# Kernel optimization log

Hardware: AMD Instinct MI355X
Metric: run time of the kernel (lower is better)

Reference implementation:

```python
import jax, jax.numpy as jnp
import numpy as np

B, T, C = 2, 2048, 2048
N_HEAD = 16
N_KV_HEAD = 16
HEAD_DIM = C // N_HEAD  # 128
KV_LORA = C // 2        # 1024
KV_PE = KV_LORA // 4    # 256
KV_CONTENT = KV_LORA - KV_PE  # 768
EPS = 1.1920929e-07  # torch.finfo(float32).eps, F.rms_norm default


def _rms_norm(x):
    # unlearned RMSNorm over last dim
    return x * jax.lax.rsqrt(jnp.mean(x * x, axis=-1, keepdims=True) + EPS)


def _apply_rotary(x, cos, sin):
    # x: (B,T,H,D); cos,sin: (1,T,1,D/2)
    d = x.shape[-1] // 2
    x1, x2 = x[..., :d], x[..., d:]
    return jnp.concatenate([x1 * cos + x2 * sin, -x1 * sin + x2 * cos], axis=-1)


def setup_inputs() -> dict:
    key = jax.random.key(0)
    ks = jax.random.split(key, 9)
    x = jax.random.normal(ks[0], (B, T, C), dtype=jnp.float32)
    # realistic RoPE tables (values bounded like real cos/sin)
    half = HEAD_DIM // 2
    inv_freq = 1.0 / (10000.0 ** (np.arange(0, half, dtype=np.float32) / half))
    tpos = np.arange(T, dtype=np.float32)
    ang = np.einsum('t,d->td', tpos, inv_freq)
    cos = jnp.asarray(np.cos(ang))[None, :, None, :]
    sin = jnp.asarray(np.sin(ang))[None, :, None, :]
    s = 0.02
    wq_a = jax.random.normal(ks[1], (C, KV_LORA), dtype=jnp.float32) * s
    wq_b = jax.random.normal(ks[2], (KV_LORA, N_HEAD * HEAD_DIM), dtype=jnp.float32) * s
    wkv_a = jax.random.normal(ks[3], (C, KV_LORA), dtype=jnp.float32) * s
    wk_b = jax.random.normal(ks[4], (KV_CONTENT, N_KV_HEAD * HEAD_DIM), dtype=jnp.float32) * s
    wkpe_b = jax.random.normal(ks[5], (KV_PE, N_KV_HEAD * HEAD_DIM), dtype=jnp.float32) * s
    wv_b = jax.random.normal(ks[6], (KV_CONTENT, N_KV_HEAD * HEAD_DIM), dtype=jnp.float32) * s
    wo = jax.random.normal(ks[7], (C, C), dtype=jnp.float32) * s
    return dict(x=x, cos=cos, sin=sin, wq_a=wq_a, wq_b=wq_b, wkv_a=wkv_a,
                wk_b=wk_b, wkpe_b=wkpe_b, wv_b=wv_b, wo=wo)


def reference(x, cos, sin, wq_a, wq_b, wkv_a, wk_b, wkpe_b, wv_b, wo):
    Bx, Tx, Cx = x.shape
    # low-rank Q path
    q = (x @ wq_a) @ wq_b                      # (B,T,H*D)
    q = q.reshape(Bx, Tx, N_HEAD, HEAD_DIM)
    # low-rank KV path with pe/content split
    kv_latent = x @ wkv_a                       # (B,T,KV_LORA)
    kv_pe = kv_latent[..., :KV_PE]
    kv_content = kv_latent[..., KV_PE:]
    k_content = (kv_content @ wk_b).reshape(Bx, Tx, N_KV_HEAD, HEAD_DIM)
    k_pe = (kv_pe @ wkpe_b).reshape(Bx, Tx, N_KV_HEAD, HEAD_DIM)
    k = k_content + _apply_rotary(k_pe, cos, sin)
    v = (kv_content @ wv_b).reshape(Bx, Tx, N_KV_HEAD, HEAD_DIM)
    # QK RMSNorm (unlearned)
    q = _rms_norm(q)
    k = _rms_norm(k)
    # SDPA, causal (kv_cache=None path); n_head == n_kv_head
    qh = q.transpose(0, 2, 1, 3)  # (B,H,T,D)
    kh = k.transpose(0, 2, 1, 3)
    vh = v.transpose(0, 2, 1, 3)
    scale = 1.0 / jnp.sqrt(jnp.asarray(HEAD_DIM, dtype=x.dtype))
    scores = jnp.einsum('bhqd,bhkd->bhqk', qh, kh) * scale
    causal = jnp.tril(jnp.ones((Tx, Tx), dtype=bool))
    scores = jnp.where(causal[None, None], scores, jnp.asarray(-jnp.inf, dtype=scores.dtype))
    probs = jax.nn.softmax(scores, axis=-1)
    y = jnp.einsum('bhqk,bhkd->bhqd', probs, vh)
    y = y.transpose(0, 2, 1, 3).reshape(Bx, Tx, Cx)
    return y @ wo
```

## Files before the change

kernel.cpp:

```cpp
#include <hip/hip_runtime.h>
#include <cstddef>
#include <cstdint>

#define TT 2048
#define HH 16
#define EPSV 1.1920929e-07f
#define QSCALE 0.08838834764831845f
#define LOG2E 1.4426950408889634f
#define THRL 11.0f

typedef short bfv8 __attribute__((ext_vector_type(8)));
typedef float f32x4 __attribute__((ext_vector_type(4)));

__device__ __forceinline__ short f2bf(float f) {
    unsigned u = __builtin_bit_cast(unsigned, f);
    u += 0x7FFFu + ((u >> 16) & 1u);
    return (short)(u >> 16);
}
__device__ __forceinline__ float bf2f(short s) {
    unsigned u = ((unsigned)(unsigned short)s) << 16;
    return __builtin_bit_cast(float, u);
}
__device__ __forceinline__ bfv8 pack8(const float4 a, const float4 b) {
    bfv8 r;
    r[0]=f2bf(a.x); r[1]=f2bf(a.y); r[2]=f2bf(a.z); r[3]=f2bf(a.w);
    r[4]=f2bf(b.x); r[5]=f2bf(b.y); r[6]=f2bf(b.z); r[7]=f2bf(b.w);
    return r;
}
__device__ __forceinline__ void gload16(const void* g, void* l) {
    __builtin_amdgcn_global_load_lds(
        (const __attribute__((address_space(1))) unsigned int*)g,
        (__attribute__((address_space(3))) unsigned int*)l, 16, 0, 0);
}

__global__ __launch_bounds__(256) void convx(const float* __restrict__ src,
                                             short* __restrict__ dst, int n8)
{
    int i = blockIdx.x * blockDim.x + threadIdx.x;
    int stride = gridDim.x * blockDim.x;
    for (; i < n8; i += stride) {
        float4 a = ((const float4*)src)[2*i], b = ((const float4*)src)[2*i+1];
        ((bfv8*)dst)[i] = pack8(a, b);
    }
}

__global__ __launch_bounds__(256) void wtrans(const float* __restrict__ src,
                                              short* __restrict__ dst, int R, int C)
{
    __shared__ short tile[64][72];
    const int tid = threadIdx.x;
    const int r0 = blockIdx.y * 64, c0 = blockIdx.x * 64;
    {
        const int i = tid >> 2, c = (tid & 3) * 16;
        const float* sp = src + ((size_t)(r0 + i)) * C + c0 + c;
        float4 v0 = ((const float4*)sp)[0], v1 = ((const float4*)sp)[1];
        float4 v2 = ((const float4*)sp)[2], v3 = ((const float4*)sp)[3];
        *(bfv8*)&tile[i][c]     = pack8(v0, v1);
        *(bfv8*)&tile[i][c + 8] = pack8(v2, v3);
    }
    __syncthreads();
    {
        const int j = tid >> 2, rc = (tid & 3) * 16;
        bfv8 g0, g1;
#pragma unroll
        for (int jj = 0; jj < 8; ++jj) { g0[jj] = tile[rc + jj][j]; g1[jj] = tile[rc + 8 + jj][j]; }
        short* dp = dst + ((size_t)(c0 + j)) * R + r0 + rc;
        *(bfv8*)dp       = g0;
        *(bfv8*)(dp + 8) = g1;
    }
}

template<int OUT_MODE>
__global__ __launch_bounds__(256) void gemm_bf16(
    const short* __restrict__ A, int lda,
    const short* __restrict__ B, int ldb,
    void* __restrict__ Cptr, int ldc, int K)
{
    __shared__ short As[2][128 * 32];
    __shared__ short Bs[2][128 * 32];
    const int tid = threadIdx.x;
    const int w = tid >> 6, lane = tid & 63;
    const int lr = lane & 15, lg = lane >> 4;
    const int wr = w >> 1, wc = w & 1;
    const size_t bm = (size_t)blockIdx.y * 128, bn = (size_t)blockIdx.x * 128;

    f32x4 acc[4][4] = {};

    const int r0 = tid >> 2, ch = (tid & 3) * 8;
    const short* aB0 = A + (bm + r0) * (size_t)lda + ch;
    const short* aB1 = aB0 + 64 * (size_t)lda;
    const short* bB0 = B + (bn + r0) * (size_t)ldb + ch;
    const short* bB1 = bB0 + 64 * (size_t)ldb;
    const int wof = w * 512;

    gload16(aB0, As[0] + wof);
    gload16(aB1, As[0] + wof + 2048);
    gload16(bB0, Bs[0] + wof);
    gload16(bB1, Bs[0] + wof + 2048);
    __syncthreads();

    int cur = 0;
    for (int k0 = 0; k0 < K; k0 += 32) {
        if (k0 + 32 < K) {
            gload16(aB0 + k0 + 32, As[cur ^ 1] + wof);
            gload16(aB1 + k0 + 32, As[cur ^ 1] + wof + 2048);
            gload16(bB0 + k0 + 32, Bs[cur ^ 1] + wof);
            gload16(bB1 + k0 + 32, Bs[cur ^ 1] + wof + 2048);
        }
        bfv8 af[4], bfr[4];
#pragma unroll
        for (int i = 0; i < 4; ++i) {
            af[i]  = *(const bfv8*)&As[cur][(wr * 64 + i * 16 + lr) * 32 + lg * 8];
            bfr[i] = *(const bfv8*)&Bs[cur][(wc * 64 + i * 16 + lr) * 32 + lg * 8];
        }
#pragma unroll
        for (int i = 0; i < 4; ++i)
#pragma unroll
            for (int j = 0; j < 4; ++j)
                acc[i][j] = __builtin_amdgcn_mfma_f32_16x16x32_bf16(af[i], bfr[j], acc[i][j], 0, 0, 0);
        __syncthreads();
        cur ^= 1;
    }

    const size_t crow = bm + wr * 64 + 4 * lg;
    const size_t ccol = bn + wc * 64 + lr;
#pragma unroll
    for (int i = 0; i < 4; ++i)
#pragma unroll
        for (int j = 0; j < 4; ++j)
#pragma unroll
            for (int r = 0; r < 4; ++r) {
                size_t off = (crow + i * 16 + r) * (size_t)ldc + ccol + j * 16;
                if (OUT_MODE == 0) ((float*)Cptr)[off] = acc[i][j][r];
                else               ((short*)Cptr)[off] = f2bf(acc[i][j][r]);
            }
}

__global__ __launch_bounds__(256) void finalize_k(
    const short* __restrict__ kc, const short* __restrict__ pe,
    const float* __restrict__ cosb, const float* __restrict__ sinb,
    short* __restrict__ kb)
{
    const int gw = blockIdx.x * 4 + (threadIdx.x >> 6);
    const int l = threadIdx.x & 63;
    const int r = gw >> 4, h = gw & 15;
    const int t = r & (TT - 1), b = r >> 11;
    const size_t kcb = (size_t)r * 4096 + h * 128;
    const size_t peb = (size_t)r * 2048 + h * 128;

    float x1 = bf2f(pe[peb + l]), x2 = bf2f(pe[peb + 64 + l]);
    float c = cosb[t * 64 + l], s = sinb[t * 64 + l];
    float lo = bf2f(kc[kcb + l])      + x1 * c + x2 * s;
    float hi = bf2f(kc[kcb + 64 + l]) - x1 * s + x2 * c;

    float ss = lo * lo + hi * hi;
#pragma unroll
    for (int o = 32; o; o >>= 1) ss += __shfl_xor(ss, o);
    float rr = rsqrtf(ss * (1.0f / 128.0f) + EPSV);
    const size_t ob = (((size_t)b * HH + h) * TT + t) * 128;
    kb[ob + l]      = f2bf(lo * rr);
    kb[ob + 64 + l] = f2bf(hi * rr);
}

__global__ __launch_bounds__(256) void finalize_q(
    const short* __restrict__ qi, short* __restrict__ qo)
{
    const int gw = blockIdx.x * 4 + (threadIdx.x >> 6);
    const int l = threadIdx.x & 63;
    const int r = gw >> 4, h = gw & 15;
    const int t = r & (TT - 1), b = r >> 11;
    const short* qp = qi + (size_t)r * 2048 + h * 128 + 2 * l;
    float a = bf2f(qp[0]), bq = bf2f(qp[1]);
    float ss = a * a + bq * bq;
#pragma unroll
    for (int o = 32; o; o >>= 1) ss += __shfl_xor(ss, o);
    float rr = rsqrtf(ss * (1.0f / 128.0f) + EPSV) * (QSCALE * LOG2E);
    short* op = qo + (((size_t)b * HH + h) * TT + t) * 128 + 2 * l;
    op[0] = f2bf(a * rr);
    op[1] = f2bf(bq * rr);
}

__global__ __launch_bounds__(256) void vtrans(
    const short* __restrict__ src, short* __restrict__ dst)
{
    __shared__ short tile[64][72];
    const int tt = blockIdx.x, dt = blockIdx.y, bh = blockIdx.z;
    const int tid = threadIdx.x;
    {
        const int i = tid >> 2, c = (tid & 3) * 16;
        const size_t sb = ((size_t)((bh >> 4) * TT + tt * 64 + i)) * 4096 + 2048 + (bh & 15) * 128 + dt * 64 + c;
        *(bfv8*)&tile[i][c]     = *(const bfv8*)&src[sb];
        *(bfv8*)&tile[i][c + 8] = *(const bfv8*)&src[sb + 8];
    }
    __syncthreads();
    {
        const int j = tid >> 2, rc = (tid & 3) * 16;
        bfv8 g0, g1;
#pragma unroll
        for (int jj = 0; jj < 8; ++jj) { g0[jj] = tile[rc + jj][j]; g1[jj] = tile[rc + 8 + jj][j]; }
        const size_t db = (((size_t)bh) * 128 + dt * 64 + j) * TT + tt * 64 + rc;
        *(bfv8*)&dst[db]     = g0;
        *(bfv8*)&dst[db + 8] = g1;
    }
}

__device__ __forceinline__ void attn_tile(
    const short* __restrict__ Ks, const short* __restrict__ Vs,
    short (&Psw)[16][72], const bfv8 aq[4], f32x4 o[8],
    float m[4], float l[4], int lr, int lg, int w, bool diag)
{
    f32x4 s[4];
#pragma unroll
    for (int ct = 0; ct < 4; ++ct) {
        f32x4 a = {0.f, 0.f, 0.f, 0.f};
        const int row = ct * 16 + lr;
#pragma unroll
        for (int ks = 0; ks < 4; ++ks) {
            const bfv8 bk = *(const bfv8*)&Ks[row * 128 + (((ks * 4 + lg) ^ (row & 7)) * 8)];
            a = __builtin_amdgcn_mfma_f32_16x16x32_bf16(aq[ks], bk, a, 0, 0, 0);
        }
        s[ct] = a;
    }
    if (diag) {
        const int rq = w * 16 + 4 * lg;
#pragma unroll
        for (int ct = 0; ct < 4; ++ct)
#pragma unroll
            for (int r = 0; r < 4; ++r)
                if (ct * 16 + lr > rq + r) s[ct][r] = -__builtin_inff();
    }
    float mt[4];
#pragma unroll
    for (int r = 0; r < 4; ++r) mt[r] = fmaxf(fmaxf(s[0][r], s[1][r]), fmaxf(s[2][r], s[3][r]));
#pragma unroll
    for (int off = 1; off < 16; off <<= 1)
#pragma unroll
        for (int r = 0; r < 4; ++r) mt[r] = fmaxf(mt[r], __shfl_xor(mt[r], off));

    float g = fmaxf(fmaxf(mt[0] - m[0], mt[1] - m[1]), fmaxf(mt[2] - m[2], mt[3] - m[3]));
    if (!__all(g <= THRL)) {
        float alpha[4];
#pragma unroll
        for (int r = 0; r < 4; ++r) {
            float mn = fmaxf(m[r], mt[r]);
            alpha[r] = exp2f(m[r] - mn);
            m[r] = mn;
            l[r] *= alpha[r];
        }
#pragma unroll
        for (int dt = 0; dt < 8; ++dt) {
            o[dt][0] *= alpha[0]; o[dt][1] *= alpha[1];
            o[dt][2] *= alpha[2]; o[dt][3] *= alpha[3];
        }
    }
#pragma unroll
    for (int ct = 0; ct < 4; ++ct)
#pragma unroll
        for (int r = 0; r < 4; ++r) s[ct][r] = exp2f(s[ct][r] - m[r]);
    float rs[4];
#pragma unroll
    for (int r = 0; r < 4; ++r) rs[r] = (s[0][r] + s[1][r]) + (s[2][r] + s[3][r]);
#pragma unroll
    for (int off = 1; off < 16; off <<= 1)
#pragma unroll
        for (int r = 0; r < 4; ++r) rs[r] += __shfl_xor(rs[r], off);
#pragma unroll
    for (int r = 0; r < 4; ++r) l[r] += rs[r];
#pragma unroll
    for (int ct = 0; ct < 4; ++ct)
#pragma unroll
        for (int r = 0; r < 4; ++r)
            Psw[4 * lg + r][ct * 16 + lr] = f2bf(s[ct][r]);
    const bfv8 pa0 = *(const bfv8*)&Psw[lr][lg * 8];
    const bfv8 pa1 = *(const bfv8*)&Psw[lr][32 + lg * 8];
#pragma unroll
    for (int dt = 0; dt < 8; ++dt) {
        const int row = dt * 16 + lr;
        const bfv8 bv0 = *(const bfv8*)&Vs[row * 64 + ((lg ^ (row & 7)) * 8)];
        const bfv8 bv1 = *(const bfv8*)&Vs[row * 64 + (((4 + lg) ^ (row & 7)) * 8)];
        o[dt] = __builtin_amdgcn_mfma_f32_16x16x32_bf16(pa0, bv0, o[dt], 0, 0, 0);
        o[dt] = __builtin_amdgcn_mfma_f32_16x16x32_bf16(pa1, bv1, o[dt], 0, 0, 0);
    }
}

__global__ __launch_bounds__(256) void attn_kernel(
    const short* __restrict__ qg, const short* __restrict__ kg,
    const short* __restrict__ vg, short* __restrict__ y)
{
    __shared__ short Ks[2][64 * 128];
    __shared__ short Vs[2][128 * 64];
    __shared__ short Ps[4][16][72];

    const int pi = blockIdx.x, h = blockIdx.y, b = blockIdx.z;
    const int qt1 = pi, qt2 = 31 - pi;
    const int tid = threadIdx.x, w = tid >> 6, lane = tid & 63;
    const int lr = lane & 15, lg = lane >> 4;

    const size_t tok0 = ((size_t)b * HH + h) * TT;
    bfv8 aq1[4], aq2[4];
    {
        const size_t q1 = (tok0 + qt1 * 64 + w * 16 + lr) * 128;
        const size_t q2 = (tok0 + qt2 * 64 + w * 16 + lr) * 128;
#pragma unroll
        for (int ks = 0; ks < 4; ++ks) {
            aq1[ks] = *(const bfv8*)&qg[q1 + ks * 32 + lg * 8];
            aq2[ks] = *(const bfv8*)&qg[q2 + ks * 32 + lg * 8];
        }
    }
    f32x4 o1[8] = {}; f32x4 o2[8] = {};
    float m1[4], l1[4], m2[4], l2[4];
#pragma unroll
    for (int r = 0; r < 4; ++r) { m1[r] = m2[r] = -__builtin_inff(); l1[r] = l2[r] = 0.f; }

    const size_t vhead = ((size_t)b * HH + h) * (size_t)128 * TT;
    const int krow = tid >> 4, kub = tid & 15;
    const int vrow = tid >> 3, vub = tid & 7;
    const int wof = w * 512;

#define STAGE_KV(KT, BUF)                                                          \
    {                                                                              \
        const size_t kbase = (tok0 + (KT) * 64) * 128;                             \
        _Pragma("unroll")                                                          \
        for (int p = 0; p < 4; ++p) {                                              \
            int row = p * 16 + krow;                                               \
            int u = kub ^ (row & 7);                                               \
            gload16(kg + kbase + row * 128 + u * 8, Ks[BUF] + wof + p * 2048);     \
            int rv = p * 32 + vrow;                                                \
            int uv = vub ^ (rv & 7);                                               \
            gload16(vg + vhead + (size_t)rv * TT + (KT) * 64 + uv * 8,             \
                    Vs[BUF] + wof + p * 2048);                                     \
        }                                                                          \
    }

    STAGE_KV(0, 0);
    __syncthreads();

    int cur = 0;
    for (int kt = 0; kt <= qt2; ++kt) {
        if (kt < qt2) STAGE_KV(kt + 1, cur ^ 1);
        attn_tile(Ks[cur], Vs[cur], Ps[w], aq2, o2, m2, l2, lr, lg, w, kt == qt2);
        if (kt <= qt1)
            attn_tile(Ks[cur], Vs[cur], Ps[w], aq1, o1, m1, l1, lr, lg, w, kt == qt1);
        __syncthreads();
        cur ^= 1;
    }

#pragma unroll
    for (int r = 0; r < 4; ++r) {
        float inv1 = 1.0f / l1[r], inv2 = 1.0f / l2[r];
        const size_t y1 = ((size_t)b * TT + qt1 * 64 + w * 16 + 4 * lg + r) * 2048 + h * 128 + lr;
        const size_t y2 = ((size_t)b * TT + qt2 * 64 + w * 16 + 4 * lg + r) * 2048 + h * 128 + lr;
#pragma unroll
        for (int dt = 0; dt < 8; ++dt) {
            y[y1 + dt * 16] = f2bf(o1[dt][r] * inv1);
            y[y2 + dt * 16] = f2bf(o2[dt][r] * inv2);
        }
    }
}

extern "C" void kernel_launch(void* const* d_in, const int* in_sizes, int n_in,
                              void* d_out, int out_size, void* d_ws, size_t ws_size,
                              hipStream_t stream)
{
    const float* x      = (const float*)d_in[0];
    const float* cosb   = (const float*)d_in[1];
    const float* sinb   = (const float*)d_in[2];
    const float* wq_a   = (const float*)d_in[3];
    const float* wq_b   = (const float*)d_in[4];
    const float* wkv_a  = (const float*)d_in[5];
    const float* wk_b   = (const float*)d_in[6];
    const float* wkpe_b = (const float*)d_in[7];
    const float* wv_b   = (const float*)d_in[8];
    const float* wo     = (const float*)d_in[9];

    short* wsp = (short*)d_ws;
    short* W1  = wsp;
    short* W2  = wsp + 4194304;
    short* W3  = wsp + 7340032;
    short* W4  = wsp + 7864320;
    short* W5  = wsp + 9961472;
    short* C1  = wsp + 14155776;
    short* KV2 = wsp + 22544384;
    short* KPE = wsp + 39321600;
    short* KB  = wsp + 47710208;
    short* VB  = wsp + 56098816;
    short* XB  = (short*)d_out;

    dim3 blk(256);

    convx<<<2048, blk, 0, stream>>>(x, XB, 1048576);
    wtrans<<<dim3(16, 32), blk, 0, stream>>>(wq_a,   W1,                2048, 1024);
    wtrans<<<dim3(16, 32), blk, 0, stream>>>(wkv_a,  W1 + 1024 * 2048,  2048, 1024);
    wtrans<<<dim3(32, 12), blk, 0, stream>>>(wk_b,   W2,                 768, 2048);
    wtrans<<<dim3(32, 12), blk, 0, stream>>>(wv_b,   W2 + 2048 * 768,    768, 2048);
    wtrans<<<dim3(32,  4), blk, 0, stream>>>(wkpe_b, W3,                 256, 2048);
    wtrans<<<dim3(32, 16), blk, 0, stream>>>(wq_b,   W4,                1024, 2048);
    wtrans<<<dim3(32, 32), blk, 0, stream>>>(wo,     W5,                2048, 2048);

    gemm_bf16<1><<<dim3(16, 32), blk, 0, stream>>>(XB, 2048, W1, 2048, C1, 2048, 2048);
    gemm_bf16<1><<<dim3(32, 32), blk, 0, stream>>>(C1 + 1280, 2048, W2, 768, KV2, 4096, 768);
    gemm_bf16<1><<<dim3(16, 32), blk, 0, stream>>>(C1 + 1024, 2048, W3, 256, KPE, 2048, 256);

    finalize_k<<<16384, blk, 0, stream>>>(KV2, KPE, cosb, sinb, KB);
    vtrans<<<dim3(32, 2, 32), blk, 0, stream>>>(KV2, VB);

    gemm_bf16<1><<<dim3(16, 32), blk, 0, stream>>>(C1, 2048, W4, 1024, KPE, 2048, 1024);
    finalize_q<<<16384, blk, 0, stream>>>(KPE, KV2);

    attn_kernel<<<dim3(16, 16, 2), blk, 0, stream>>>(KV2, KB, VB, C1);

    gemm_bf16<0><<<dim3(16, 32), blk, 0, stream>>>(C1, 2048, W5, 2048, d_out, 2048, 2048);
}
```

Baseline: 374.9 us.

## Interleave QK, softmax and PV of paired query tiles and remap block order

Splits the attention tile routine into separate QK, masking, softmax and PV stages. For key tiles shared by both query tiles, the two QK products, the two softmax reductions and the two PV products are issued back to back, so independent MFMA and shuffle chains can overlap. The causal loop is split into a phase with both tiles and a phase with only the later tile, which removes the per-iteration branch. Block indices are also remapped so that consecutive hardware blocks are spread across heads and batches, aiming for better load balance and cache use. Keeping both tiles' scores live raises register pressure and may lower occupancy.

```diff
diff --git a/kernel.cpp b/kernel.cpp
--- a/kernel.cpp
+++ b/kernel.cpp
@@ -204,12 +204,9 @@
     }
 }
 
-__device__ __forceinline__ void attn_tile(
-    const short* __restrict__ Ks, const short* __restrict__ Vs,
-    short (&Psw)[16][72], const bfv8 aq[4], f32x4 o[8],
-    float m[4], float l[4], int lr, int lg, int w, bool diag)
-{
-    f32x4 s[4];
+__device__ __forceinline__ void qk_tile(const short* __restrict__ Ks,
+    const bfv8 aq[4], f32x4 s[4], int lr, int lg)
+{
 #pragma unroll
     for (int ct = 0; ct < 4; ++ct) {
         f32x4 a = {0.f, 0.f, 0.f, 0.f};
@@ -221,14 +218,20 @@
         }
         s[ct] = a;
     }
-    if (diag) {
-        const int rq = w * 16 + 4 * lg;
-#pragma unroll
-        for (int ct = 0; ct < 4; ++ct)
-#pragma unroll
-            for (int r = 0; r < 4; ++r)
-                if (ct * 16 + lr > rq + r) s[ct][r] = -__builtin_inff();
-    }
+}
+
+__device__ __forceinline__ void mask_diag(f32x4 s[4], int lr, int lg, int w)
+{
+    const int rq = w * 16 + 4 * lg;
+#pragma unroll
+    for (int ct = 0; ct < 4; ++ct)
+#pragma unroll
+        for (int r = 0; r < 4; ++r)
+            if (ct * 16 + lr > rq + r) s[ct][r] = -__builtin_inff();
+}
+
+__device__ __forceinline__ void softmax1(f32x4 s[4], float m[4], float l[4], f32x4 o[8])
+{
     float mt[4];
 #pragma unroll
     for (int r = 0; r < 4; ++r) mt[r] = fmaxf(fmaxf(s[0][r], s[1][r]), fmaxf(s[2][r], s[3][r]));
@@ -236,7 +239,6 @@
     for (int off = 1; off < 16; off <<= 1)
 #pragma unroll
         for (int r = 0; r < 4; ++r) mt[r] = fmaxf(mt[r], __shfl_xor(mt[r], off));
-
     float g = fmaxf(fmaxf(mt[0] - m[0], mt[1] - m[1]), fmaxf(mt[2] - m[2], mt[3] - m[3]));
     if (!__all(g <= THRL)) {
         float alpha[4];
@@ -244,8 +246,7 @@
         for (int r = 0; r < 4; ++r) {
             float mn = fmaxf(m[r], mt[r]);
             alpha[r] = exp2f(m[r] - mn);
-            m[r] = mn;
-            l[r] *= alpha[r];
+            m[r] = mn; l[r] *= alpha[r];
         }
 #pragma unroll
         for (int dt = 0; dt < 8; ++dt) {
@@ -266,6 +267,83 @@
         for (int r = 0; r < 4; ++r) rs[r] += __shfl_xor(rs[r], off);
 #pragma unroll
     for (int r = 0; r < 4; ++r) l[r] += rs[r];
+}
+
+__device__ __forceinline__ void softmax2(
+    f32x4 s1[4], f32x4 s2[4],
+    float m1[4], float l1[4], float m2[4], float l2[4],
+    f32x4 o1[8], f32x4 o2[8])
+{
+    float mt1[4], mt2[4];
+#pragma unroll
+    for (int r = 0; r < 4; ++r) {
+        mt1[r] = fmaxf(fmaxf(s1[0][r], s1[1][r]), fmaxf(s1[2][r], s1[3][r]));
+        mt2[r] = fmaxf(fmaxf(s2[0][r], s2[1][r]), fmaxf(s2[2][r], s2[3][r]));
+    }
+#pragma unroll
+    for (int off = 1; off < 16; off <<= 1)
+#pragma unroll
+        for (int r = 0; r < 4; ++r) {
+            mt1[r] = fmaxf(mt1[r], __shfl_xor(mt1[r], off));
+            mt2[r] = fmaxf(mt2[r], __shfl_xor(mt2[r], off));
+        }
+    float g1 = fmaxf(fmaxf(mt1[0] - m1[0], mt1[1] - m1[1]), fmaxf(mt1[2] - m1[2], mt1[3] - m1[3]));
+    float g2 = fmaxf(fmaxf(mt2[0] - m2[0], mt2[1] - m2[1]), fmaxf(mt2[2] - m2[2], mt2[3] - m2[3]));
+    if (!__all(g1 <= THRL)) {
+        float alpha[4];
+#pragma unroll
+        for (int r = 0; r < 4; ++r) {
+            float mn = fmaxf(m1[r], mt1[r]);
+            alpha[r] = exp2f(m1[r] - mn);
+            m1[r] = mn; l1[r] *= alpha[r];
+        }
+#pragma unroll
+        for (int dt = 0; dt < 8; ++dt) {
+            o1[dt][0] *= alpha[0]; o1[dt][1] *= alpha[1];
+            o1[dt][2] *= alpha[2]; o1[dt][3] *= alpha[3];
+        }
+    }
+    if (!__all(g2 <= THRL)) {
+        float alpha[4];
+#pragma unroll
+        for (int r = 0; r < 4; ++r) {
+            float mn = fmaxf(m2[r], mt2[r]);
+            alpha[r] = exp2f(m2[r] - mn);
+            m2[r] = mn; l2[r] *= alpha[r];
+        }
+#pragma unroll
+        for (int dt = 0; dt < 8; ++dt) {
+            o2[dt][0] *= alpha[0]; o2[dt][1] *= alpha[1];
+            o2[dt][2] *= alpha[2]; o2[dt][3] *= alpha[3];
+        }
+    }
+#pragma unroll
+    for (int ct = 0; ct < 4; ++ct)
+#pragma unroll
+        for (int r = 0; r < 4; ++r) {
+            s1[ct][r] = exp2f(s1[ct][r] - m1[r]);
+            s2[ct][r] = exp2f(s2[ct][r] - m2[r]);
+        }
+    float rs1[4], rs2[4];
+#pragma unroll
+    for (int r = 0; r < 4; ++r) {
+        rs1[r] = (s1[0][r] + s1[1][r]) + (s1[2][r] + s1[3][r]);
+        rs2[r] = (s2[0][r] + s2[1][r]) + (s2[2][r] + s2[3][r]);
+    }
+#pragma unroll
+    for (int off = 1; off < 16; off <<= 1)
+#pragma unroll
+        for (int r = 0; r < 4; ++r) {
+            rs1[r] += __shfl_xor(rs1[r], off);
+            rs2[r] += __shfl_xor(rs2[r], off);
+        }
+#pragma unroll
+    for (int r = 0; r < 4; ++r) { l1[r] += rs1[r]; l2[r] += rs2[r]; }
+}
+
+__device__ __forceinline__ void pv_tile(const short* __restrict__ Vs,
+    short (&Psw)[16][72], const f32x4 s[4], f32x4 o[8], int lr, int lg)
+{
 #pragma unroll
     for (int ct = 0; ct < 4; ++ct)
 #pragma unroll
@@ -291,7 +369,9 @@
     __shared__ short Vs[2][128 * 64];
     __shared__ short Ps[4][16][72];
 
-    const int pi = blockIdx.x, h = blockIdx.y, b = blockIdx.z;
+    const int lin = blockIdx.x + 16 * blockIdx.y + 256 * blockIdx.z;
+    const int work = (lin & 7) * 64 + (lin >> 3);
+    const int pi = work & 15, h = (work >> 4) & 15, b = work >> 8;
     const int qt1 = pi, qt2 = 31 - pi;
     const int tid = threadIdx.x, w = tid >> 6, lane = tid & 63;
     const int lr = lane & 15, lg = lane >> 4;
@@ -336,11 +416,25 @@
     __syncthreads();
 
     int cur = 0;
-    for (int kt = 0; kt <= qt2; ++kt) {
+    for (int kt = 0; kt <= qt1; ++kt) {
         if (kt < qt2) STAGE_KV(kt + 1, cur ^ 1);
-        attn_tile(Ks[cur], Vs[cur], Ps[w], aq2, o2, m2, l2, lr, lg, w, kt == qt2);
-        if (kt <= qt1)
-            attn_tile(Ks[cur], Vs[cur], Ps[w], aq1, o1, m1, l1, lr, lg, w, kt == qt1);
+        f32x4 s1[4], s2[4];
+        qk_tile(Ks[cur], aq2, s2, lr, lg);
+        qk_tile(Ks[cur], aq1, s1, lr, lg);
+        if (kt == qt1) mask_diag(s1, lr, lg, w);
+        softmax2(s1, s2, m1, l1, m2, l2, o1, o2);
+        pv_tile(Vs[cur], Ps[w], s2, o2, lr, lg);
+        pv_tile(Vs[cur], Ps[w], s1, o1, lr, lg);
+        __syncthreads();
+        cur ^= 1;
+    }
+    for (int kt = qt1 + 1; kt <= qt2; ++kt) {
+        if (kt < qt2) STAGE_KV(kt + 1, cur ^ 1);
+        f32x4 s2[4];
+        qk_tile(Ks[cur], aq2, s2, lr, lg);
+        if (kt == qt2) mask_diag(s2, lr, lg, w);
+        softmax1(s2, m2, l2, o2);
+        pv_tile(Vs[cur], Ps[w], s2, o2, lr, lg);
         __syncthreads();
         cur ^= 1;
     }
```

Result: faster. 357.1 us (-4.8%).
